# Performance work log

Measured on AMD Instinct MI355X. Metric: run time of the kernel, lower is better.

## Reference

```python
import jax, jax.numpy as jnp
import numpy as np

B, T, D = 2, 2048, 1024
G, E, F = 4, 4, 4096          # num_groups, experts_per_group, d_ff
KG, KE = 2, 1                  # top_k_groups, top_k_experts


def setup_inputs() -> dict:
    key = jax.random.key(0)
    ks = jax.random.split(key, 5)
    init = lambda k, shape, fan: jax.random.normal(k, shape, jnp.float32) / np.sqrt(fan).astype(np.float32)
    x = jax.random.normal(ks[0], (B, T, D), jnp.float32)
    Wg = init(ks[1], (G, D), D)          # group router (torch Linear weight [out,in])
    We = init(ks[2], (G, E, D), D)       # per-group expert routers
    W1 = init(ks[3], (G, E, F, D), D)    # expert up-proj weights
    W2 = init(ks[4], (G, E, D, F), F)    # expert down-proj weights
    return {"x": x, "Wg": Wg, "We": We, "W1": W1, "W2": W2}


def _moe_forward(x, Wg, We, W1, W2):
    b, t, d = x.shape
    xf = x.reshape(b * t, d)                                   # [N, D]
    group_logits = xf @ Wg.T                                   # [N, G]
    gw, gid = jax.lax.top_k(group_logits, KG)                  # [N, KG]
    gw = jax.nn.softmax(gw, axis=-1)
    expert_logits = jnp.einsum('nd,ged->nge', xf, We)          # [N, G, E]
    sel = jnp.take_along_axis(expert_logits, gid[:, :, None], axis=1)  # [N, KG, E]
    ew, eid = jax.lax.top_k(sel, KE)                           # [N, KG, KE]
    ew = jax.nn.softmax(ew, axis=-1)
    w = gw[:, :, None] * ew                                    # [N, KG, KE]
    oh_g = jax.nn.one_hot(gid, G, dtype=xf.dtype)              # [N, KG, G]
    oh_e = jax.nn.one_hot(eid, E, dtype=xf.dtype)              # [N, KG, KE, E]
    # topk group ids are distinct, and expert ids within a group are distinct,
    # so this scatter-by-one-hot exactly reproduces the masked accumulation.
    combine = jnp.einsum('nrg,nrke,nrk->nge', oh_g, oh_e, w)   # [N, G, E]
    out = jnp.zeros_like(xf)
    for g in range(G):
        for e in range(E):
            h = jax.nn.gelu(xf @ W1[g, e].T, approximate=False)  # exact GELU, as nn.GELU()
            out = out + combine[:, g, e, None] * (h @ W2[g, e].T)
    return out.reshape(b, t, d), group_logits.reshape(b, t, G)


def reference(x, Wg, We, W1, W2):
    out, group_logits = _moe_forward(x, Wg, We, W1, W2)
    p = jax.nn.softmax(group_logits, axis=-1)
    lp = jax.nn.log_softmax(group_logits, axis=-1)
    group_entropy = -(p * lp).sum(-1).mean()
    return out, group_logits, group_entropy
```

## Files before the change

kernel.cpp:

```cpp
#include <hip/hip_runtime.h>
#include <hip/hip_bf16.h>

#define NTOK 4096
#define DDIM 1024
#define GG 4
#define EE 4
#define FF 4096
#define NEXP 16
#define MAXTILES 80
#define OUT_ELEMS 4194304
#define GL_OFF 4194304
#define ENT_OFF 4210688

typedef float f32x4 __attribute__((ext_vector_type(4)));
typedef short short8 __attribute__((ext_vector_type(8)));

__device__ inline unsigned short f2bf(float f) {
  unsigned int u = __float_as_uint(f);
  unsigned int rounding = 0x7FFFu + ((u >> 16) & 1u);
  return (unsigned short)((u + rounding) >> 16);
}
__device__ inline unsigned int pack2(float f0, float f1) {
  return (unsigned int)f2bf(f0) | ((unsigned int)f2bf(f1) << 16);
}
__device__ inline unsigned int pack2rn(float f0, float f1) {
  unsigned int u0 = __float_as_uint(f0), u1 = __float_as_uint(f1);
  return ((u0 + 0x8000u) >> 16) | ((u1 + 0x8000u) & 0xFFFF0000u);
}

__device__ __forceinline__ void gload_lds16(const void* g, void* l) {
  __builtin_amdgcn_global_load_lds(
      (const __attribute__((address_space(1))) unsigned int*)g,
      (__attribute__((address_space(3))) unsigned int*)l, 16, 0, 0);
}

__global__ __launch_bounds__(256) void routing_kernel(
    const float* __restrict__ x, const float* __restrict__ Wg,
    const float* __restrict__ We, float* __restrict__ out,
    int* __restrict__ cnt, int* __restrict__ tokL, int* __restrict__ hrwL,
    float* __restrict__ wslot, unsigned short* __restrict__ xb,
    float* __restrict__ entPart) {
  int wave = threadIdx.x >> 6, lane = threadIdx.x & 63;
  int token = blockIdx.x * 4 + wave;
  const float4* xr = reinterpret_cast<const float4*>(x + (size_t)token * DDIM);
  float4 xv[4];
#pragma unroll
  for (int c = 0; c < 4; c++) xv[c] = xr[c * 64 + lane];

  {
    uint2* xbr = reinterpret_cast<uint2*>(xb + (size_t)token * DDIM);
#pragma unroll
    for (int c = 0; c < 4; c++) {
      uint2 pv;
      pv.x = pack2(xv[c].x, xv[c].y);
      pv.y = pack2(xv[c].z, xv[c].w);
      xbr[c * 64 + lane] = pv;
    }
  }

  auto dotrow = [&](const float* w) -> float {
    const float4* w4 = reinterpret_cast<const float4*>(w);
    float s = 0.f;
#pragma unroll
    for (int c = 0; c < 4; c++) {
      float4 wv = w4[c * 64 + lane];
      s += xv[c].x * wv.x + xv[c].y * wv.y + xv[c].z * wv.z + xv[c].w * wv.w;
    }
#pragma unroll
    for (int off = 32; off; off >>= 1) s += __shfl_xor(s, off, 64);
    return s;
  };

  float gl[GG];
#pragma unroll
  for (int g = 0; g < GG; g++) gl[g] = dotrow(Wg + g * DDIM);

  int g0 = 0;
  for (int g = 1; g < GG; g++) if (gl[g] > gl[g0]) g0 = g;
  int g1 = -1;
  for (int g = 0; g < GG; g++) { if (g == g0) continue; if (g1 < 0 || gl[g] > gl[g1]) g1 = g; }
  float e1 = __expf(gl[g1] - gl[g0]);
  float inv = 1.f / (1.f + e1);
  float w0 = inv, w1 = e1 * inv;

  int gsel[2] = {g0, g1};
  float wsel[2] = {w0, w1};
  int esel[2];
#pragma unroll
  for (int r = 0; r < 2; r++) {
    float el[EE];
#pragma unroll
    for (int e = 0; e < EE; e++) el[e] = dotrow(We + ((size_t)gsel[r] * EE + e) * DDIM);
    int best = 0;
    for (int e = 1; e < EE; e++) if (el[e] > el[best]) best = e;
    esel[r] = best;
  }

  float m = gl[0];
  for (int g = 1; g < GG; g++) m = fmaxf(m, gl[g]);
  float se = 0.f;
  for (int g = 0; g < GG; g++) se += __expf(gl[g] - m);
  float lse = __logf(se);
  float ent = 0.f;
  for (int g = 0; g < GG; g++) {
    float lp = gl[g] - m - lse;
    ent -= __expf(lp) * lp;
  }

  __shared__ float entS[4];
  if (lane == 0) {
    entS[wave] = ent;
    for (int g = 0; g < GG; g++) out[GL_OFF + token * GG + g] = gl[g];
    for (int r = 0; r < 2; r++) {
      int ge = gsel[r] * EE + esel[r];
      int pos = atomicAdd(cnt + ge, 1);
      tokL[ge * NTOK + pos] = token;
      hrwL[ge * NTOK + pos] = r * NTOK + token;
      wslot[r * NTOK + token] = wsel[r];
    }
  }
  __syncthreads();
  if (threadIdx.x == 0)
    entPart[blockIdx.x] = entS[0] + entS[1] + entS[2] + entS[3];
}

__global__ void ent_finalize(const float* __restrict__ entPart,
                             float* __restrict__ out) {
  int t = threadIdx.x;
  float s = 0.f;
  for (int i = t; i < 1024; i += 256) s += entPart[i];
#pragma unroll
  for (int off = 32; off; off >>= 1) s += __shfl_xor(s, off, 64);
  __shared__ float ws4[4];
  if ((t & 63) == 0) ws4[t >> 6] = s;
  __syncthreads();
  if (t == 0) out[ENT_OFF] = (ws4[0] + ws4[1] + ws4[2] + ws4[3]) * (1.0f / NTOK);
}

template <int KDIM, bool UP>
__global__ __launch_bounds__(256, 2) void moe_gemm(
    const unsigned short* __restrict__ A, const float* __restrict__ W,
    const int* __restrict__ cnt, const int* __restrict__ tokL,
    const int* __restrict__ hrwL, unsigned short* __restrict__ Hout,
    float* __restrict__ Yout) {
  constexpr int NT = KDIM / 64;
  constexpr int NROWS = UP ? FF : DDIM;
  int ge = -1, mt = 0;
  {
    int y = blockIdx.y, a = 0;
    for (int g = 0; g < NEXP; g++) {
      int ntl = (cnt[g] + 127) >> 7;
      if (y < a + ntl) { ge = g; mt = y - a; break; }
      a += ntl;
    }
  }
  if (ge < 0) return;
  int count = cnt[ge];
  int n0 = blockIdx.x * 128;

  __shared__ alignas(16) unsigned short As[2][128 * 64];
  __shared__ alignas(16) unsigned short Bs[2][128 * 64];
  __shared__ int srcS[128];
  __shared__ int dstS[128];

  int t = threadIdx.x;
  int w = t >> 6, lane = t & 63;
  if (t < 128) {
    int i = mt * 128 + t;
    bool valid = i < count;
    int hrw = valid ? hrwL[ge * NTOK + i] : -1;
    dstS[t] = hrw;
    if (UP) srcS[t] = valid ? tokL[ge * NTOK + i] : 0;
    else    srcS[t] = hrw < 0 ? 0 : hrw;
  }
  __syncthreads();

  int cA = (lane & 7) ^ (lane >> 3);
  const unsigned short* gA[4];
#pragma unroll
  for (int c = 0; c < 4; c++)
    gA[c] = A + (size_t)srcS[w * 32 + c * 8 + (lane >> 3)] * KDIM + cA * 8;

  int rB = t >> 3, cB = t & 7;
  const float* gB = W + ((size_t)ge * NROWS + n0 + rB) * KDIM + cB * 8;
  int pB = (cB ^ (rB & 7)) * 8;

  int wr = w >> 1, wc = w & 1;
  int m0 = wr * 64, nw = wc * 64;
  int rl = lane & 15, kq = lane >> 4;
  int xr = rl & 7;

  f32x4 acc[4][4] = {};
  int cur = 0;

  {
    float4 q[8];
#pragma unroll
    for (int qq = 0; qq < 4; qq++) {
      q[qq * 2]     = *reinterpret_cast<const float4*>(gB + (size_t)(qq * 32) * KDIM);
      q[qq * 2 + 1] = *reinterpret_cast<const float4*>(gB + (size_t)(qq * 32) * KDIM + 4);
    }
#pragma unroll
    for (int c = 0; c < 4; c++)
      gload_lds16(gA[c], &As[0][(w * 32 + c * 8) * 64]);
#pragma unroll
    for (int qq = 0; qq < 4; qq++) {
      uint4 v;
      v.x = pack2rn(q[qq * 2].x, q[qq * 2].y);
      v.y = pack2rn(q[qq * 2].z, q[qq * 2].w);
      v.z = pack2rn(q[qq * 2 + 1].x, q[qq * 2 + 1].y);
      v.w = pack2rn(q[qq * 2 + 1].z, q[qq * 2 + 1].w);
      *reinterpret_cast<uint4*>(&Bs[0][(rB + qq * 32) * 64 + pB]) = v;
    }
  }
  __syncthreads();

  for (int it = 0; it < NT; ++it) {
    int kb = (it + 1) * 64;
    bool pre = (it + 1) < NT;
    float4 q[8];
    if (pre) {
#pragma unroll
      for (int qq = 0; qq < 4; qq++) {
        q[qq * 2]     = *reinterpret_cast<const float4*>(gB + (size_t)(qq * 32) * KDIM + kb);
        q[qq * 2 + 1] = *reinterpret_cast<const float4*>(gB + (size_t)(qq * 32) * KDIM + kb + 4);
      }
#pragma unroll
      for (int c = 0; c < 4; c++)
        gload_lds16(gA[c] + kb, &As[cur ^ 1][(w * 32 + c * 8) * 64]);
    }
    const unsigned short* Ab = As[cur];
    const unsigned short* Bb = Bs[cur];
#pragma unroll
    for (int kk = 0; kk < 2; kk++) {
      int cph = ((kk * 4 + kq) ^ xr) * 8;
      short8 af[4];
#pragma unroll
      for (int i = 0; i < 4; i++)
        af[i] = *reinterpret_cast<const short8*>(&Ab[(m0 + i * 16 + rl) * 64 + cph]);
#pragma unroll
      for (int j = 0; j < 4; j++) {
        short8 bf = *reinterpret_cast<const short8*>(&Bb[(nw + j * 16 + rl) * 64 + cph]);
#pragma unroll
        for (int i = 0; i < 4; i++)
          acc[i][j] = __builtin_amdgcn_mfma_f32_16x16x32_bf16(af[i], bf, acc[i][j], 0, 0, 0);
      }
    }
    if (pre) {
#pragma unroll
      for (int qq = 0; qq < 4; qq++) {
        uint4 v;
        v.x = pack2rn(q[qq * 2].x, q[qq * 2].y);
        v.y = pack2rn(q[qq * 2].z, q[qq * 2].w);
        v.z = pack2rn(q[qq * 2 + 1].x, q[qq * 2 + 1].y);
        v.w = pack2rn(q[qq * 2 + 1].z, q[qq * 2 + 1].w);
        *reinterpret_cast<uint4*>(&Bs[cur ^ 1][(rB + qq * 32) * 64 + pB]) = v;
      }
    }
    __syncthreads();
    cur ^= 1;
  }

  int re = kq * 4;
#pragma unroll
  for (int i = 0; i < 4; i++) {
#pragma unroll
    for (int e = 0; e < 4; e++) {
      int hr = dstS[m0 + i * 16 + re + e];
      if (hr >= 0) {
        if constexpr (UP) {
#pragma unroll
          for (int j = 0; j < 4; j++) {
            float v = acc[i][j][e];
            float gel = 0.5f * v * (1.0f + erff(v * 0.70710678118654752f));
            Hout[(size_t)hr * FF + n0 + nw + j * 16 + rl] = f2bf(gel);
          }
        } else {
#pragma unroll
          for (int j = 0; j < 4; j++)
            Yout[(size_t)hr * DDIM + n0 + nw + j * 16 + rl] = acc[i][j][e];
        }
      }
    }
  }
}

__global__ void combine_kernel(const float* __restrict__ Y,
                               const float* __restrict__ wslot,
                               float* __restrict__ out) {
  int idx = blockIdx.x * 256 + threadIdx.x;
  int token = idx >> 8;
  float w0 = wslot[token], w1 = wslot[NTOK + token];
  float4 a = reinterpret_cast<const float4*>(Y)[idx];
  float4 b = reinterpret_cast<const float4*>(Y + (size_t)NTOK * DDIM)[idx];
  float4 o;
  o.x = w0 * a.x + w1 * b.x;
  o.y = w0 * a.y + w1 * b.y;
  o.z = w0 * a.z + w1 * b.z;
  o.w = w0 * a.w + w1 * b.w;
  reinterpret_cast<float4*>(out)[idx] = o;
}

extern "C" void kernel_launch(void* const* d_in, const int* in_sizes, int n_in,
                              void* d_out, int out_size, void* d_ws, size_t ws_size,
                              hipStream_t stream) {
  const float* x  = (const float*)d_in[0];
  const float* Wg = (const float*)d_in[1];
  const float* We = (const float*)d_in[2];
  const float* W1 = (const float*)d_in[3];
  const float* W2 = (const float*)d_in[4];
  float* out = (float*)d_out;
  char* ws = (char*)d_ws;

  int* cnt = (int*)(ws);
  int* tokL = (int*)(ws + 1024);
  int* hrwL = (int*)(ws + 1024 + 262144);
  float* wslot = (float*)(ws + 1024 + 524288);
  float* entPart = (float*)(ws + 1024 + 524288 + 32768);
  unsigned short* xb = (unsigned short*)(ws + (1 << 20));
  unsigned short* H  = (unsigned short*)(ws + (1 << 20) + 8388608);
  float* Y = (float*)(ws + (1 << 20) + 8388608 + 67108864);

  hipMemsetAsync(d_out, 0, (size_t)out_size * sizeof(float), stream);
  hipMemsetAsync(ws, 0, 1024, stream);

  routing_kernel<<<1024, 256, 0, stream>>>(x, Wg, We, out, cnt, tokL, hrwL,
                                           wslot, xb, entPart);
  moe_gemm<DDIM, true><<<dim3(FF / 128, MAXTILES), 256, 0, stream>>>(
      xb, W1, cnt, tokL, hrwL, H, nullptr);
  moe_gemm<FF, false><<<dim3(DDIM / 128, MAXTILES), 256, 0, stream>>>(
      H, W2, cnt, tokL, hrwL, nullptr, Y);
  combine_kernel<<<4096, 256, 0, stream>>>(Y, wslot, out);
  ent_finalize<<<1, 256, 0, stream>>>(entPart, out);
}
```

Measured before the change: 1.032 ms.

## Use 512-thread blocks with deeper manual prefetch pipeline in MoE GEMM

```diff
diff --git a/kernel.cpp b/kernel.cpp
--- a/kernel.cpp
+++ b/kernel.cpp
@@ -138,7 +138,7 @@
 }
 
 template <int KDIM, bool UP>
-__global__ __launch_bounds__(256, 2) void moe_gemm(
+__global__ __launch_bounds__(512, 4) void moe_gemm(
     const unsigned short* __restrict__ A, const float* __restrict__ W,
     const int* __restrict__ cnt, const int* __restrict__ tokL,
     const int* __restrict__ hrwL, unsigned short* __restrict__ Hout,
@@ -175,95 +175,101 @@
   }
   __syncthreads();
 
+  int rA = w * 16 + (lane >> 3);
   int cA = (lane & 7) ^ (lane >> 3);
-  const unsigned short* gA[4];
-#pragma unroll
-  for (int c = 0; c < 4; c++)
-    gA[c] = A + (size_t)srcS[w * 32 + c * 8 + (lane >> 3)] * KDIM + cA * 8;
+  const unsigned short* gA0 = A + (size_t)srcS[rA] * KDIM + cA * 8;
+  const unsigned short* gA1 = A + (size_t)srcS[rA + 8] * KDIM + cA * 8;
 
   int rB = t >> 3, cB = t & 7;
-  const float* gB = W + ((size_t)ge * NROWS + n0 + rB) * KDIM + cB * 8;
+  const float* gB0 = W + ((size_t)ge * NROWS + n0 + rB) * KDIM + cB * 8;
+  const float* gB1 = W + ((size_t)ge * NROWS + n0 + 64 + rB) * KDIM + cB * 8;
   int pB = (cB ^ (rB & 7)) * 8;
 
   int wr = w >> 1, wc = w & 1;
-  int m0 = wr * 64, nw = wc * 64;
+  int m0 = wr * 32, nw = wc * 64;
   int rl = lane & 15, kq = lane >> 4;
   int xr = rl & 7;
 
-  f32x4 acc[4][4] = {};
-  int cur = 0;
-
-  {
-    float4 q[8];
-#pragma unroll
-    for (int qq = 0; qq < 4; qq++) {
-      q[qq * 2]     = *reinterpret_cast<const float4*>(gB + (size_t)(qq * 32) * KDIM);
-      q[qq * 2 + 1] = *reinterpret_cast<const float4*>(gB + (size_t)(qq * 32) * KDIM + 4);
-    }
-#pragma unroll
-    for (int c = 0; c < 4; c++)
-      gload_lds16(gA[c], &As[0][(w * 32 + c * 8) * 64]);
-#pragma unroll
-    for (int qq = 0; qq < 4; qq++) {
-      uint4 v;
-      v.x = pack2rn(q[qq * 2].x, q[qq * 2].y);
-      v.y = pack2rn(q[qq * 2].z, q[qq * 2].w);
-      v.z = pack2rn(q[qq * 2 + 1].x, q[qq * 2 + 1].y);
-      v.w = pack2rn(q[qq * 2 + 1].z, q[qq * 2 + 1].w);
-      *reinterpret_cast<uint4*>(&Bs[0][(rB + qq * 32) * 64 + pB]) = v;
-    }
-  }
-  __syncthreads();
-
-  for (int it = 0; it < NT; ++it) {
-    int kb = (it + 1) * 64;
-    bool pre = (it + 1) < NT;
-    float4 q[8];
-    if (pre) {
-#pragma unroll
-      for (int qq = 0; qq < 4; qq++) {
-        q[qq * 2]     = *reinterpret_cast<const float4*>(gB + (size_t)(qq * 32) * KDIM + kb);
-        q[qq * 2 + 1] = *reinterpret_cast<const float4*>(gB + (size_t)(qq * 32) * KDIM + kb + 4);
-      }
-#pragma unroll
-      for (int c = 0; c < 4; c++)
-        gload_lds16(gA[c] + kb, &As[cur ^ 1][(w * 32 + c * 8) * 64]);
-    }
-    const unsigned short* Ab = As[cur];
-    const unsigned short* Bb = Bs[cur];
+  f32x4 acc[2][4] = {};
+  float4 qa[4], qb[4];
+
+  auto loadB = [&](float4* q, int kb) {
+    q[0] = *reinterpret_cast<const float4*>(gB0 + kb);
+    q[1] = *reinterpret_cast<const float4*>(gB0 + kb + 4);
+    q[2] = *reinterpret_cast<const float4*>(gB1 + kb);
+    q[3] = *reinterpret_cast<const float4*>(gB1 + kb + 4);
+  };
+  auto packB = [&](const float4* q, unsigned short* buf) {
+    uint4 v0, v1;
+    v0.x = pack2rn(q[0].x, q[0].y); v0.y = pack2rn(q[0].z, q[0].w);
+    v0.z = pack2rn(q[1].x, q[1].y); v0.w = pack2rn(q[1].z, q[1].w);
+    v1.x = pack2rn(q[2].x, q[2].y); v1.y = pack2rn(q[2].z, q[2].w);
+    v1.z = pack2rn(q[3].x, q[3].y); v1.w = pack2rn(q[3].z, q[3].w);
+    *reinterpret_cast<uint4*>(&buf[rB * 64 + pB]) = v0;
+    *reinterpret_cast<uint4*>(&buf[(rB + 64) * 64 + pB]) = v1;
+  };
+  auto stageA = [&](int buf, int kb) {
+    gload_lds16(gA0 + kb, &As[buf][(w * 16) * 64]);
+    gload_lds16(gA1 + kb, &As[buf][(w * 16 + 8) * 64]);
+  };
+  auto compute = [&](const unsigned short* Ab, const unsigned short* Bb) {
 #pragma unroll
     for (int kk = 0; kk < 2; kk++) {
       int cph = ((kk * 4 + kq) ^ xr) * 8;
-      short8 af[4];
-#pragma unroll
-      for (int i = 0; i < 4; i++)
-        af[i] = *reinterpret_cast<const short8*>(&Ab[(m0 + i * 16 + rl) * 64 + cph]);
+      short8 af0 = *reinterpret_cast<const short8*>(&Ab[(m0 + rl) * 64 + cph]);
+      short8 af1 = *reinterpret_cast<const short8*>(&Ab[(m0 + 16 + rl) * 64 + cph]);
 #pragma unroll
       for (int j = 0; j < 4; j++) {
         short8 bf = *reinterpret_cast<const short8*>(&Bb[(nw + j * 16 + rl) * 64 + cph]);
-#pragma unroll
-        for (int i = 0; i < 4; i++)
-          acc[i][j] = __builtin_amdgcn_mfma_f32_16x16x32_bf16(af[i], bf, acc[i][j], 0, 0, 0);
+        acc[0][j] = __builtin_amdgcn_mfma_f32_16x16x32_bf16(af0, bf, acc[0][j], 0, 0, 0);
+        acc[1][j] = __builtin_amdgcn_mfma_f32_16x16x32_bf16(af1, bf, acc[1][j], 0, 0, 0);
       }
     }
-    if (pre) {
-#pragma unroll
-      for (int qq = 0; qq < 4; qq++) {
-        uint4 v;
-        v.x = pack2rn(q[qq * 2].x, q[qq * 2].y);
-        v.y = pack2rn(q[qq * 2].z, q[qq * 2].w);
-        v.z = pack2rn(q[qq * 2 + 1].x, q[qq * 2 + 1].y);
-        v.w = pack2rn(q[qq * 2 + 1].z, q[qq * 2 + 1].w);
-        *reinterpret_cast<uint4*>(&Bs[cur ^ 1][(rB + qq * 32) * 64 + pB]) = v;
-      }
-    }
-    __syncthreads();
-    cur ^= 1;
+  };
+
+  loadB(qa, 0);
+  stageA(0, 0);
+  __builtin_amdgcn_sched_barrier(0);
+  loadB(qb, 64);
+  packB(qa, Bs[0]);
+  asm volatile("s_waitcnt vmcnt(4) lgkmcnt(0)" ::: "memory");
+  __builtin_amdgcn_s_barrier();
+  __builtin_amdgcn_sched_barrier(0);
+
+  for (int it = 0; it < NT; it += 2) {
+    {
+      int tt = it;
+      stageA(1, (tt + 1) * 64);
+      __builtin_amdgcn_sched_barrier(0);
+      if (tt + 2 < NT) loadB(qa, (tt + 2) * 64);
+      compute(As[0], Bs[0]);
+      packB(qb, Bs[1]);
+      if (tt + 2 < NT)
+        asm volatile("s_waitcnt vmcnt(4) lgkmcnt(0)" ::: "memory");
+      else
+        asm volatile("s_waitcnt vmcnt(0) lgkmcnt(0)" ::: "memory");
+      __builtin_amdgcn_s_barrier();
+      __builtin_amdgcn_sched_barrier(0);
+    }
+    {
+      int tt = it + 1;
+      if (tt + 1 < NT) stageA(0, (tt + 1) * 64);
+      __builtin_amdgcn_sched_barrier(0);
+      if (tt + 2 < NT) loadB(qb, (tt + 2) * 64);
+      compute(As[1], Bs[1]);
+      if (tt + 1 < NT) packB(qa, Bs[0]);
+      if (tt + 2 < NT)
+        asm volatile("s_waitcnt vmcnt(4) lgkmcnt(0)" ::: "memory");
+      else
+        asm volatile("s_waitcnt vmcnt(0) lgkmcnt(0)" ::: "memory");
+      __builtin_amdgcn_s_barrier();
+      __builtin_amdgcn_sched_barrier(0);
+    }
   }
 
   int re = kq * 4;
 #pragma unroll
-  for (int i = 0; i < 4; i++) {
+  for (int i = 0; i < 2; i++) {
 #pragma unroll
     for (int e = 0; e < 4; e++) {
       int hr = dstS[m0 + i * 16 + re + e];
@@ -326,9 +332,9 @@
 
   routing_kernel<<<1024, 256, 0, stream>>>(x, Wg, We, out, cnt, tokL, hrwL,
                                            wslot, xb, entPart);
-  moe_gemm<DDIM, true><<<dim3(FF / 128, MAXTILES), 256, 0, stream>>>(
+  moe_gemm<DDIM, true><<<dim3(FF / 128, MAXTILES), 512, 0, stream>>>(
       xb, W1, cnt, tokL, hrwL, H, nullptr);
-  moe_gemm<FF, false><<<dim3(DDIM / 128, MAXTILES), 256, 0, stream>>>(
+  moe_gemm<FF, false><<<dim3(DDIM / 128, MAXTILES), 512, 0, stream>>>(
       H, W2, cnt, tokL, hrwL, nullptr, Y);
   combine_kernel<<<4096, 256, 0, stream>>>(Y, wslot, out);
   ent_finalize<<<1, 256, 0, stream>>>(entPart, out);
```

After: 975.0 us. -5.5%, faster.
